# Optimization experiments

Hardware: AMD Instinct MI355X
Metric: run time of the kernel (lower is better)

The kernel has to match this reference:

```python
import jax, jax.numpy as jnp
import numpy as np

B, S, D, H = 2, 2048, 2048, 16
HD = D // H  # head_dim = 128
ALIBI_BIAS_MAX = 8


def alibi_bias(n_heads, seq_len, alibi_bias_max=8, dtype=jnp.float32):
    # matches torch alibi_bias(full=False): shape [1, H, 1, S]
    dist = jnp.arange(1 - seq_len, 1, dtype=dtype).reshape(1, 1, 1, seq_len)
    m = jnp.arange(1, n_heads + 1, dtype=dtype) * (alibi_bias_max / n_heads)
    slopes = (1.0 / 2.0 ** m).reshape(1, n_heads, 1, 1)
    return dist * slopes


def setup_inputs() -> dict:
    key = jax.random.key(0)
    k1, k2, k3, k4, k5 = jax.random.split(key, 5)
    x = jax.random.normal(k1, (B, S, D), dtype=jnp.float32)
    # ALiBi additive bias, as produced by TritonFlashCausalAttention.attn_mask_
    attn_mask = alibi_bias(H, S, ALIBI_BIAS_MAX, jnp.float32)  # [1,H,1,S]
    scale = 1.0 / np.sqrt(D)
    Wqkv = jax.random.normal(k2, (D, 3 * D), dtype=jnp.float32) * scale
    bqkv = jnp.zeros((3 * D,), dtype=jnp.float32)
    Wout = jax.random.normal(k3, (D, D), dtype=jnp.float32) * scale
    bout = jnp.zeros((D,), dtype=jnp.float32)
    return {"x": x, "attn_mask": attn_mask, "Wqkv": Wqkv, "bqkv": bqkv,
            "Wout": Wout, "bout": bout}


def reference(x, attn_mask, Wqkv, bqkv, Wout, bout):
    b, s, d = x.shape
    # fused QKV projection
    qkv = x @ Wqkv + bqkv                       # [B,S,3D]
    qkv = qkv.reshape(b, s, 3, H, HD)
    q, k, v = qkv[:, :, 0], qkv[:, :, 1], qkv[:, :, 2]  # each [B,S,H,HD]
    softmax_scale = 1.0 / jnp.sqrt(jnp.asarray(HD, dtype=x.dtype))
    scores = jnp.einsum('bshd,bthd->bhst', q, k) * softmax_scale  # [B,H,S,S]
    scores = scores + attn_mask                  # ALiBi bias [1,H,1,S]
    causal = jnp.tril(jnp.ones((s, s), dtype=bool))
    scores = jnp.where(causal, scores, jnp.asarray(-jnp.inf, dtype=scores.dtype))
    attn = jax.nn.softmax(scores, axis=-1)
    out = jnp.einsum('bhst,bthd->bshd', attn, v).reshape(b, s, d)
    return out @ Wout + bout
```

## Files before the change

### kernel.cpp

```cpp
#include <hip/hip_runtime.h>
#include <hip/hip_bf16.h>

typedef __bf16 bf16x8 __attribute__((ext_vector_type(8)));
typedef float f32x4 __attribute__((ext_vector_type(4)));
typedef unsigned short u16;

constexpr int BATCH = 2, SEQ = 2048, DM = 2048, NH = 16, HD = 128;
constexpr int N3 = 3 * DM;
constexpr int MROWS = BATCH * SEQ;

__device__ __forceinline__ u16 f2bf(float f) {
  unsigned u = __builtin_bit_cast(unsigned, f);
  unsigned r = 0x7FFFu + ((u >> 16) & 1u);
  return (u16)((u + r) >> 16);
}

__device__ __forceinline__ void glds16(const u16* g, u16* l) {
  __builtin_amdgcn_global_load_lds(
      (const __attribute__((address_space(1))) unsigned*)(const void*)g,
      (__attribute__((address_space(3))) unsigned*)(void*)l, 16, 0, 0);
}

__global__ __launch_bounds__(256) void k_cvt(const float* __restrict__ in,
                                             u16* __restrict__ out, int n4) {
  int i = blockIdx.x * blockDim.x + threadIdx.x;
  if (i >= n4) return;
  float4 v = reinterpret_cast<const float4*>(in)[i];
  ushort4 o;
  o.x = f2bf(v.x); o.y = f2bf(v.y); o.z = f2bf(v.z); o.w = f2bf(v.w);
  reinterpret_cast<ushort4*>(out)[i] = o;
}

__global__ __launch_bounds__(256) void k_transpose(const float* __restrict__ in,
                                                   u16* __restrict__ out, int K, int N) {
  __shared__ float tile[32][33];
  int n0 = blockIdx.x * 32, k0 = blockIdx.y * 32;
  int tx = threadIdx.x & 31, ty = threadIdx.x >> 5;
#pragma unroll
  for (int r = ty; r < 32; r += 8) tile[r][tx] = in[(long)(k0 + r) * N + n0 + tx];
  __syncthreads();
#pragma unroll
  for (int r = ty; r < 32; r += 8) out[(long)(n0 + r) * K + k0 + tx] = f2bf(tile[tx][r]);
}

__global__ __launch_bounds__(256) void k_gemm_qkv(const u16* __restrict__ A,
                                                  const u16* __restrict__ Bt,
                                                  const float* __restrict__ bias,
                                                  u16* __restrict__ Qb, u16* __restrict__ Kb,
                                                  u16* __restrict__ Vt) {
  constexpr int K = DM;
  __shared__ u16 As[128 * 32], Bs[128 * 32];
  int m0 = blockIdx.y * 128, n0 = blockIdx.x * 128;
  int t = threadIdx.x, lane = t & 63, w = t >> 6;
  int l15 = lane & 15, lhi = lane >> 4;
  int wr = (w >> 1) * 64, wc = (w & 1) * 64;
  int srow = t >> 2, sk = (t & 3) * 8;
  const u16* Ap0 = A + (long)(m0 + srow) * K + sk;
  const u16* Ap1 = A + (long)(m0 + 64 + srow) * K + sk;
  const u16* Bp0 = Bt + (long)(n0 + srow) * K + sk;
  const u16* Bp1 = Bt + (long)(n0 + 64 + srow) * K + sk;
  u16* AsW0 = As + w * 512; u16* AsW1 = As + 2048 + w * 512;
  u16* BsW0 = Bs + w * 512; u16* BsW1 = Bs + 2048 + w * 512;

  f32x4 acc[4][4] = {};
  for (int k0 = 0; k0 < K; k0 += 32) {
    glds16(Ap0 + k0, AsW0);
    glds16(Ap1 + k0, AsW1);
    glds16(Bp0 + k0, BsW0);
    glds16(Bp1 + k0, BsW1);
    __syncthreads();
    bf16x8 af[4], bg[4];
#pragma unroll
    for (int i = 0; i < 4; i++) af[i] = *(const bf16x8*)(As + (wr + i * 16 + l15) * 32 + lhi * 8);
#pragma unroll
    for (int j = 0; j < 4; j++) bg[j] = *(const bf16x8*)(Bs + (wc + j * 16 + l15) * 32 + lhi * 8);
#pragma unroll
    for (int i = 0; i < 4; i++)
#pragma unroll
      for (int j = 0; j < 4; j++)
        acc[i][j] = __builtin_amdgcn_mfma_f32_16x16x32_bf16(af[i], bg[j], acc[i][j], 0, 0, 0);
    __syncthreads();
  }
#pragma unroll
  for (int i = 0; i < 4; i++)
#pragma unroll
    for (int j = 0; j < 4; j++) {
      int col = n0 + wc + j * 16 + l15;
      float bv = bias[col];
      int sec = col >> 11, dn = col & 2047, h = dn >> 7, hd = dn & 127;
#pragma unroll
      for (int r = 0; r < 4; r++) {
        int row = m0 + wr + i * 16 + lhi * 4 + r;
        int bb = row >> 11, ss = row & 2047;
        u16 val = f2bf(acc[i][j][r] + bv);
        if (sec == 0)
          Qb[(((long)(bb * NH + h)) * SEQ + ss) * HD + hd] = val;
        else if (sec == 1)
          Kb[(((long)(bb * NH + h)) * SEQ + ss) * HD + hd] = val;
        else
          Vt[(((long)(bb * NH + h)) * HD + hd) * SEQ + ss] = val;
      }
    }
}

__global__ __launch_bounds__(256) void k_gemm_out(const u16* __restrict__ A,
                                                  const u16* __restrict__ Bt,
                                                  const float* __restrict__ bias,
                                                  float* __restrict__ Out) {
  constexpr int K = DM, N = DM;
  __shared__ u16 As[128 * 32], Bs[128 * 32];
  int m0 = blockIdx.y * 128, n0 = blockIdx.x * 128;
  int t = threadIdx.x, lane = t & 63, w = t >> 6;
  int l15 = lane & 15, lhi = lane >> 4;
  int wr = (w >> 1) * 64, wc = (w & 1) * 64;
  int srow = t >> 2, sk = (t & 3) * 8;
  const u16* Ap0 = A + (long)(m0 + srow) * K + sk;
  const u16* Ap1 = A + (long)(m0 + 64 + srow) * K + sk;
  const u16* Bp0 = Bt + (long)(n0 + srow) * K + sk;
  const u16* Bp1 = Bt + (long)(n0 + 64 + srow) * K + sk;
  u16* AsW0 = As + w * 512; u16* AsW1 = As + 2048 + w * 512;
  u16* BsW0 = Bs + w * 512; u16* BsW1 = Bs + 2048 + w * 512;

  f32x4 acc[4][4] = {};
  for (int k0 = 0; k0 < K; k0 += 32) {
    glds16(Ap0 + k0, AsW0);
    glds16(Ap1 + k0, AsW1);
    glds16(Bp0 + k0, BsW0);
    glds16(Bp1 + k0, BsW1);
    __syncthreads();
    bf16x8 af[4], bg[4];
#pragma unroll
    for (int i = 0; i < 4; i++) af[i] = *(const bf16x8*)(As + (wr + i * 16 + l15) * 32 + lhi * 8);
#pragma unroll
    for (int j = 0; j < 4; j++) bg[j] = *(const bf16x8*)(Bs + (wc + j * 16 + l15) * 32 + lhi * 8);
#pragma unroll
    for (int i = 0; i < 4; i++)
#pragma unroll
      for (int j = 0; j < 4; j++)
        acc[i][j] = __builtin_amdgcn_mfma_f32_16x16x32_bf16(af[i], bg[j], acc[i][j], 0, 0, 0);
    __syncthreads();
  }
#pragma unroll
  for (int i = 0; i < 4; i++)
#pragma unroll
    for (int j = 0; j < 4; j++) {
      int col = n0 + wc + j * 16 + l15;
      float bv = bias[col];
#pragma unroll
      for (int r = 0; r < 4; r++) {
        int row = m0 + wr + i * 16 + lhi * 4 + r;
        Out[(long)row * N + col] = acc[i][j][r] + bv;
      }
    }
}

__global__ __launch_bounds__(256) void k_attn(const u16* __restrict__ Qb,
                                              const u16* __restrict__ Kb,
                                              const u16* __restrict__ Vt,
                                              const float* __restrict__ mask,
                                              u16* __restrict__ Ao) {
  constexpr int NT = SEQ / 64;
  int bh = blockIdx.y;
  int qp = blockIdx.x;
  int t = threadIdx.x, w = t >> 6, lane = t & 63;
  int l15 = lane & 15, lhi = lane >> 4;
  int b = bh >> 4, h = bh & 15;
  const u16* Qh = Qb + (long)bh * SEQ * HD;
  const u16* Kh = Kb + (long)bh * SEQ * HD;
  const u16* Vh = Vt + (long)bh * HD * SEQ;
  const float* mh = mask + h * SEQ;

  __shared__ u16 Ks[64 * 128];
  __shared__ u16 Vs[128 * 64];
  __shared__ u16 p_lds[4 * 16 * 64];
  u16* pw = p_lds + w * (16 * 64);

  int krow[4], kcol[4], vrow[4], vcol[4];
#pragma unroll
  for (int i = 0; i < 4; i++) {
    int c = i * 256 + t;
    krow[i] = c >> 4; kcol[i] = (c & 15) * 8;
    vrow[i] = c >> 3; vcol[i] = (c & 7) * 8;
  }

  const float sm_scale = 0.08838834764831845f;

  for (int half = 0; half < 2; half++) {
    int qt = half ? qp : (NT - 1 - qp);
    int q0 = qt * 64 + w * 16;
    int nt = qt + 1;

    bf16x8 qf[4];
#pragma unroll
    for (int kc = 0; kc < 4; kc++)
      qf[kc] = *(const bf16x8*)(Qh + (long)(q0 + l15) * HD + kc * 32 + lhi * 8);

    int rowr[4];
#pragma unroll
    for (int r = 0; r < 4; r++) rowr[r] = q0 + lhi * 4 + r;

    float mrun[4], lrun[4];
    f32x4 oacc[8] = {};
#pragma unroll
    for (int r = 0; r < 4; r++) { mrun[r] = -1e30f; lrun[r] = 0.f; }

    bf16x8 kst[4], vst[4];
#pragma unroll
    for (int i = 0; i < 4; i++) kst[i] = *(const bf16x8*)(Kh + (long)krow[i] * HD + kcol[i]);
#pragma unroll
    for (int i = 0; i < 4; i++) vst[i] = *(const bf16x8*)(Vh + (long)vrow[i] * SEQ + vcol[i]);
    __syncthreads();
#pragma unroll
    for (int i = 0; i < 4; i++)
      *(bf16x8*)(Ks + krow[i] * 128 + (kcol[i] ^ ((krow[i] & 7) << 3))) = kst[i];
#pragma unroll
    for (int i = 0; i < 4; i++)
      *(bf16x8*)(Vs + vrow[i] * 64 + (vcol[i] ^ ((vrow[i] & 7) << 3))) = vst[i];
    __syncthreads();

    for (int kt = 0; kt < nt; kt++) {
      int kb = kt * 64;
      bool have_next = (kt + 1 < nt);
      bool diag = (kt == nt - 1);
      if (have_next) {
        int kb2 = kb + 64;
#pragma unroll
        for (int i = 0; i < 4; i++)
          kst[i] = *(const bf16x8*)(Kh + (long)(kb2 + krow[i]) * HD + kcol[i]);
#pragma unroll
        for (int i = 0; i < 4; i++)
          vst[i] = *(const bf16x8*)(Vh + (long)vrow[i] * SEQ + kb2 + vcol[i]);
      }
      float bvv[4];
#pragma unroll
      for (int cb = 0; cb < 4; cb++) bvv[cb] = mh[kb + cb * 16 + l15];
      f32x4 sc[4] = {};
      __builtin_amdgcn_s_setprio(1);
#pragma unroll
      for (int kc = 0; kc < 4; kc++)
#pragma unroll
        for (int cb = 0; cb < 4; cb++) {
          int rr = cb * 16 + l15;
          bf16x8 kf = *(const bf16x8*)(Ks + rr * 128 + ((kc * 32 + lhi * 8) ^ ((rr & 7) << 3)));
          sc[cb] = __builtin_amdgcn_mfma_f32_16x16x32_bf16(qf[kc], kf, sc[cb], 0, 0, 0);
        }
      __builtin_amdgcn_s_setprio(0);
      float p[4][4], tmax[4];
#pragma unroll
      for (int cb = 0; cb < 4; cb++) {
        int col = kb + cb * 16 + l15;
#pragma unroll
        for (int r = 0; r < 4; r++) {
          float v = sc[cb][r] * sm_scale + bvv[cb];
          if (diag) v = (col <= rowr[r]) ? v : -1e30f;
          p[cb][r] = v;
        }
      }
#pragma unroll
      for (int r = 0; r < 4; r++)
        tmax[r] = fmaxf(fmaxf(p[0][r], p[1][r]), fmaxf(p[2][r], p[3][r]));
      float alpha[4];
#pragma unroll
      for (int r = 0; r < 4; r++) {
        float v = tmax[r];
        v = fmaxf(v, __shfl_xor(v, 1));
        v = fmaxf(v, __shfl_xor(v, 2));
        v = fmaxf(v, __shfl_xor(v, 4));
        v = fmaxf(v, __shfl_xor(v, 8));
        float mnew = fmaxf(mrun[r], v);
        alpha[r] = __expf(mrun[r] - mnew);
        mrun[r] = mnew;
        float s = 0.f;
#pragma unroll
        for (int cb = 0; cb < 4; cb++) {
          float e = __expf(p[cb][r] - mnew);
          p[cb][r] = e;
          s += e;
        }
        s += __shfl_xor(s, 1); s += __shfl_xor(s, 2);
        s += __shfl_xor(s, 4); s += __shfl_xor(s, 8);
        lrun[r] = lrun[r] * alpha[r] + s;
      }
#pragma unroll
      for (int nb = 0; nb < 8; nb++)
#pragma unroll
        for (int r = 0; r < 4; r++) oacc[nb][r] *= alpha[r];
#pragma unroll
      for (int cb = 0; cb < 4; cb++)
#pragma unroll
        for (int r = 0; r < 4; r++) {
          int rr = lhi * 4 + r;
          pw[(rr * 64 + cb * 16 + l15) ^ ((rr & 7) << 3)] = f2bf(p[cb][r]);
        }
      asm volatile("s_waitcnt lgkmcnt(0)" ::: "memory");
      bf16x8 pa0 = *(const bf16x8*)(pw + ((l15 * 64 + lhi * 8) ^ ((l15 & 7) << 3)));
      bf16x8 pa1 = *(const bf16x8*)(pw + ((l15 * 64 + 32 + lhi * 8) ^ ((l15 & 7) << 3)));
      __builtin_amdgcn_s_setprio(1);
#pragma unroll
      for (int nb = 0; nb < 8; nb++) {
        int rr = nb * 16 + l15;
        bf16x8 vf0 = *(const bf16x8*)(Vs + rr * 64 + ((lhi * 8) ^ ((rr & 7) << 3)));
        bf16x8 vf1 = *(const bf16x8*)(Vs + rr * 64 + ((32 + lhi * 8) ^ ((rr & 7) << 3)));
        oacc[nb] = __builtin_amdgcn_mfma_f32_16x16x32_bf16(pa0, vf0, oacc[nb], 0, 0, 0);
        oacc[nb] = __builtin_amdgcn_mfma_f32_16x16x32_bf16(pa1, vf1, oacc[nb], 0, 0, 0);
      }
      __builtin_amdgcn_s_setprio(0);
      if (have_next) {
        __syncthreads();
#pragma unroll
        for (int i = 0; i < 4; i++)
          *(bf16x8*)(Ks + krow[i] * 128 + (kcol[i] ^ ((krow[i] & 7) << 3))) = kst[i];
#pragma unroll
        for (int i = 0; i < 4; i++)
          *(bf16x8*)(Vs + vrow[i] * 64 + (vcol[i] ^ ((vrow[i] & 7) << 3))) = vst[i];
        __syncthreads();
      }
    }
#pragma unroll
    for (int nb = 0; nb < 8; nb++)
#pragma unroll
      for (int r = 0; r < 4; r++) {
        int row = q0 + lhi * 4 + r;
        float v = oacc[nb][r] / lrun[r];
        Ao[((long)(b * SEQ + row)) * DM + h * HD + nb * 16 + l15] = f2bf(v);
      }
  }
}

extern "C" void kernel_launch(void* const* d_in, const int* in_sizes, int n_in,
                              void* d_out, int out_size, void* d_ws, size_t ws_size,
                              hipStream_t stream) {
  const float* x    = (const float*)d_in[0];
  const float* amsk = (const float*)d_in[1];
  const float* Wqkv = (const float*)d_in[2];
  const float* bqkv = (const float*)d_in[3];
  const float* Wout = (const float*)d_in[4];
  const float* bout = (const float*)d_in[5];
  float* out = (float*)d_out;

  char* ws = (char*)d_ws;
  u16* xb  = (u16*)(ws + 0);
  u16* WqT = (u16*)(ws + 16777216UL);
  u16* WoT = (u16*)(ws + 41943040UL);
  u16* Qb  = (u16*)(ws + 50331648UL);
  u16* Kb  = (u16*)(ws + 67108864UL);
  u16* Vt  = (u16*)(ws + 83886080UL);
  u16* Ao  = (u16*)(ws + 100663296UL);

  k_cvt<<<8192, 256, 0, stream>>>(x, xb, (MROWS * DM) / 4);
  k_transpose<<<dim3(N3 / 32, DM / 32), 256, 0, stream>>>(Wqkv, WqT, DM, N3);
  k_transpose<<<dim3(DM / 32, DM / 32), 256, 0, stream>>>(Wout, WoT, DM, DM);
  k_gemm_qkv<<<dim3(N3 / 128, MROWS / 128), 256, 0, stream>>>(xb, WqT, bqkv, Qb, Kb, Vt);
  k_attn<<<dim3(SEQ / 128, BATCH * NH), 256, 0, stream>>>(Qb, Kb, Vt, amsk, Ao);
  k_gemm_out<<<dim3(DM / 128, MROWS / 128), 256, 0, stream>>>(Ao, WoT, bout, out);
}
```

Before: 310.8 us.

## Rewrite QKV GEMM with 256x256 tiles, double-buffered LDS and swizzle

The QKV projection GEMM moves from 128x128 tiles with 256 threads to 256x256 tiles with 512 threads and a BK of 64. Shared-memory loads are double-buffered and interleaved with MFMA phases, with explicit vmcnt waits and barriers. An XOR swizzle avoids LDS bank conflicts, and s_setprio raises priority around the MFMA blocks. The aim is to hide global-load latency and raise operand reuse per block. In exchange it uses far more LDS (128KB) and registers, and the grid drops to 24x16 blocks.

```diff
diff --git a/kernel.cpp b/kernel.cpp
--- a/kernel.cpp
+++ b/kernel.cpp
@@ -43,56 +43,101 @@
   for (int r = ty; r < 32; r += 8) out[(long)(n0 + r) * K + k0 + tx] = f2bf(tile[tx][r]);
 }
 
-__global__ __launch_bounds__(256) void k_gemm_qkv(const u16* __restrict__ A,
+__global__ __launch_bounds__(512) void k_gemm_qkv(const u16* __restrict__ A,
                                                   const u16* __restrict__ Bt,
                                                   const float* __restrict__ bias,
                                                   u16* __restrict__ Qb, u16* __restrict__ Kb,
                                                   u16* __restrict__ Vt) {
   constexpr int K = DM;
-  __shared__ u16 As[128 * 32], Bs[128 * 32];
-  int m0 = blockIdx.y * 128, n0 = blockIdx.x * 128;
+  constexpr int NKT = K / 64;
+  constexpr int NIT = NKT / 2;
+  __shared__ u16 LA[2 * 256 * 64];
+  __shared__ u16 LB[2 * 256 * 64];
+  int m0 = blockIdx.y * 256, n0 = blockIdx.x * 256;
   int t = threadIdx.x, lane = t & 63, w = t >> 6;
   int l15 = lane & 15, lhi = lane >> 4;
-  int wr = (w >> 1) * 64, wc = (w & 1) * 64;
-  int srow = t >> 2, sk = (t & 3) * 8;
-  const u16* Ap0 = A + (long)(m0 + srow) * K + sk;
-  const u16* Ap1 = A + (long)(m0 + 64 + srow) * K + sk;
-  const u16* Bp0 = Bt + (long)(n0 + srow) * K + sk;
-  const u16* Bp1 = Bt + (long)(n0 + 64 + srow) * K + sk;
-  u16* AsW0 = As + w * 512; u16* AsW1 = As + 2048 + w * 512;
-  u16* BsW0 = Bs + w * 512; u16* BsW1 = Bs + 2048 + w * 512;
-
-  f32x4 acc[4][4] = {};
-  for (int k0 = 0; k0 < K; k0 += 32) {
-    glds16(Ap0 + k0, AsW0);
-    glds16(Ap1 + k0, AsW1);
-    glds16(Bp0 + k0, BsW0);
-    glds16(Bp1 + k0, BsW1);
-    __syncthreads();
-    bf16x8 af[4], bg[4];
-#pragma unroll
-    for (int i = 0; i < 4; i++) af[i] = *(const bf16x8*)(As + (wr + i * 16 + l15) * 32 + lhi * 8);
-#pragma unroll
-    for (int j = 0; j < 4; j++) bg[j] = *(const bf16x8*)(Bs + (wc + j * 16 + l15) * 32 + lhi * 8);
-#pragma unroll
-    for (int i = 0; i < 4; i++)
-#pragma unroll
-      for (int j = 0; j < 4; j++)
-        acc[i][j] = __builtin_amdgcn_mfma_f32_16x16x32_bf16(af[i], bg[j], acc[i][j], 0, 0, 0);
-    __syncthreads();
+  int wrow = w >> 2, wcol = w & 3;
+  int srow = t >> 3;
+  int scol = ((t & 7) ^ (srow & 7)) * 8;
+
+#define STG_A(TILE, HALF) do {                                                   \
+    int kb_ = ((TILE) < NKT ? (TILE) : NKT - 1) * 64;                            \
+    u16* d_ = LA + (((TILE) & 1) * 16384 + (HALF) * 8192 + w * 512);             \
+    glds16(A + (long)(m0 + (HALF) * 128 + srow) * K + kb_ + scol, d_);           \
+    glds16(A + (long)(m0 + (HALF) * 128 + 64 + srow) * K + kb_ + scol, d_ + 4096); \
+  } while (0)
+#define STG_B(TILE, HALF) do {                                                   \
+    int kb_ = ((TILE) < NKT ? (TILE) : NKT - 1) * 64;                            \
+    u16* d_ = LB + (((TILE) & 1) * 16384 + (HALF) * 8192 + w * 512);             \
+    glds16(Bt + (long)(n0 + (HALF) * 128 + srow) * K + kb_ + scol, d_);          \
+    glds16(Bt + (long)(n0 + (HALF) * 128 + 64 + srow) * K + kb_ + scol, d_ + 4096); \
+  } while (0)
+
+  bf16x8 af[4][2], bfr[4][2];
+  f32x4 acc[8][4] = {};
+
+#define LDA_FRAGS(BUF, QM) do {                                                  \
+    _Pragma("unroll") for (int mi = 0; mi < 4; mi++) {                           \
+      int rA = wrow * 128 + ((QM) * 4 + mi) * 16 + l15;                          \
+      _Pragma("unroll") for (int kk = 0; kk < 2; kk++)                           \
+        af[mi][kk] = *(const bf16x8*)(LA + (BUF) * 16384 + rA * 64 +             \
+                                      (((kk * 4 + lhi) ^ (rA & 7)) * 8));        \
+    } } while (0)
+#define LDB_FRAGS(BUF, QN) do {                                                  \
+    _Pragma("unroll") for (int ni = 0; ni < 2; ni++) {                           \
+      int rB = wcol * 64 + ((QN) * 2 + ni) * 16 + l15;                           \
+      _Pragma("unroll") for (int kk = 0; kk < 2; kk++)                           \
+        bfr[(QN) * 2 + ni][kk] = *(const bf16x8*)(LB + (BUF) * 16384 + rB * 64 + \
+                                      (((kk * 4 + lhi) ^ (rB & 7)) * 8));        \
+    } } while (0)
+#define MM(QM, QN) do {                                                          \
+    __builtin_amdgcn_s_setprio(1);                                               \
+    _Pragma("unroll") for (int mi = 0; mi < 4; mi++)                             \
+    _Pragma("unroll") for (int ni = 0; ni < 2; ni++)                             \
+    _Pragma("unroll") for (int kk = 0; kk < 2; kk++)                             \
+      acc[(QM) * 4 + mi][(QN) * 2 + ni] = __builtin_amdgcn_mfma_f32_16x16x32_bf16( \
+          af[mi][kk], bfr[(QN) * 2 + ni][kk], acc[(QM) * 4 + mi][(QN) * 2 + ni], 0, 0, 0); \
+    __builtin_amdgcn_s_setprio(0);                                               \
+  } while (0)
+#define BAR __builtin_amdgcn_s_barrier()
+#define VMW4 do { asm volatile("s_waitcnt vmcnt(4)" ::: "memory");               \
+                  __builtin_amdgcn_sched_barrier(0); } while (0)
+
+  STG_A(0, 0); STG_A(0, 1); STG_B(0, 0); STG_B(0, 1);
+  STG_B(1, 0); STG_B(1, 1);
+  VMW4; BAR;
+
+  for (int it = 0; it < NIT; it++) {
+    int k1 = 2 * it + 1, k2 = 2 * it + 2, k3 = 2 * it + 3;
+    LDA_FRAGS(0, 0); LDB_FRAGS(0, 0); STG_A(k1, 0);       BAR; MM(0, 0); BAR;
+    LDB_FRAGS(0, 1);                  STG_A(k1, 1);       BAR; MM(0, 1); BAR;
+    LDA_FRAGS(0, 1);                  STG_B(k2, 0);       BAR; MM(1, 0); BAR;
+                                      STG_B(k2, 1); VMW4; BAR; MM(1, 1); BAR;
+    LDA_FRAGS(1, 0); LDB_FRAGS(1, 0); STG_A(k2, 0);       BAR; MM(0, 0); BAR;
+    LDB_FRAGS(1, 1);                  STG_A(k2, 1);       BAR; MM(0, 1); BAR;
+    LDA_FRAGS(1, 1);                  STG_B(k3, 0);       BAR; MM(1, 0); BAR;
+                                      STG_B(k3, 1); VMW4; BAR; MM(1, 1); BAR;
   }
-#pragma unroll
-  for (int i = 0; i < 4; i++)
-#pragma unroll
-    for (int j = 0; j < 4; j++) {
-      int col = n0 + wc + j * 16 + l15;
+#undef STG_A
+#undef STG_B
+#undef LDA_FRAGS
+#undef LDB_FRAGS
+#undef MM
+#undef BAR
+#undef VMW4
+
+#pragma unroll
+  for (int mi = 0; mi < 8; mi++)
+#pragma unroll
+    for (int ni = 0; ni < 4; ni++) {
+      int col = n0 + wcol * 64 + ni * 16 + l15;
       float bv = bias[col];
       int sec = col >> 11, dn = col & 2047, h = dn >> 7, hd = dn & 127;
 #pragma unroll
       for (int r = 0; r < 4; r++) {
-        int row = m0 + wr + i * 16 + lhi * 4 + r;
+        int row = m0 + wrow * 128 + mi * 16 + lhi * 4 + r;
         int bb = row >> 11, ss = row & 2047;
-        u16 val = f2bf(acc[i][j][r] + bv);
+        u16 val = f2bf(acc[mi][ni][r] + bv);
         if (sec == 0)
           Qb[(((long)(bb * NH + h)) * SEQ + ss) * HD + hd] = val;
         else if (sec == 1)
@@ -350,7 +395,7 @@
   k_cvt<<<8192, 256, 0, stream>>>(x, xb, (MROWS * DM) / 4);
   k_transpose<<<dim3(N3 / 32, DM / 32), 256, 0, stream>>>(Wqkv, WqT, DM, N3);
   k_transpose<<<dim3(DM / 32, DM / 32), 256, 0, stream>>>(Wout, WoT, DM, DM);
-  k_gemm_qkv<<<dim3(N3 / 128, MROWS / 128), 256, 0, stream>>>(xb, WqT, bqkv, Qb, Kb, Vt);
+  k_gemm_qkv<<<dim3(N3 / 256, MROWS / 256), 512, 0, stream>>>(xb, WqT, bqkv, Qb, Kb, Vt);
   k_attn<<<dim3(SEQ / 128, BATCH * NH), 256, 0, stream>>>(Qb, Kb, Vt, amsk, Ao);
   k_gemm_out<<<dim3(DM / 128, MROWS / 128), 256, 0, stream>>>(Ao, WoT, bout, out);
 }
```

Result: slower. 325.6 us (+4.8%).
